# Performance work log

Measured on AMD Instinct MI355X. Metric: run time of the kernel, lower is better.

The kernel has to match this reference:

```python
import jax, jax.numpy as jnp
import numpy as np


def setup_inputs() -> dict:
    key = jax.random.key(0)
    k1, k2, k3 = jax.random.split(key, 3)
    x = jax.random.normal(k1, (32, 256, 56, 56), dtype=jnp.float32)
    att_w = jax.random.normal(k2, (4, 256), dtype=jnp.float32) * 0.05  # 1x1 attention conv weight (K, Cin)
    weight = jax.random.normal(k3, (4, 256, 256, 3, 3), dtype=jnp.float32) * 0.05  # (K, Cout, Cin, kh, kw)
    return {"x": x, "att_w": att_w, "weight": weight}


def reference(x, att_w, weight):
    # x: (B, Cin, H, W); att_w: (K, Cin); weight: (K, Cout, Cin, kh, kw)
    # Attention: global avg pool -> 1x1 conv (Cin->K) -> sigmoid  (named softmax_att but is sigmoid)
    pooled = jnp.mean(x, axis=(2, 3))                 # (B, Cin)
    att = jax.nn.sigmoid(pooled @ att_w.T)            # (B, K)
    # Per-sample expert-mixed conv kernels
    agg_w = jnp.einsum('bk,koihw->boihw', att, weight)  # (B, Cout, Cin, kh, kw)

    def conv_one(xi, wi):
        # xi: (Cin, H, W), wi: (Cout, Cin, kh, kw)
        return jax.lax.conv_general_dilated(
            xi[None], wi,
            window_strides=(1, 1),
            padding=[(1, 1), (1, 1)],
            rhs_dilation=(1, 1),
            dimension_numbers=('NCHW', 'OIHW', 'NCHW'),
        )[0]

    out = jax.vmap(conv_one)(x, agg_w)                # (B, Cout, H, W)
    return out
```

## Files before the change

kernel.cpp:

```cpp
#include <hip/hip_runtime.h>

typedef __attribute__((ext_vector_type(8))) short short8;
typedef __attribute__((ext_vector_type(4))) float floatx4;

__device__ __forceinline__ unsigned short bf16_rne(float f) {
  unsigned int u = __builtin_bit_cast(unsigned int, f);
  u += 0x7fffu + ((u >> 16) & 1u);
  return (unsigned short)(u >> 16);
}

__device__ __forceinline__ void glds16(const void* g, void* l) {
  __builtin_amdgcn_global_load_lds((const __attribute__((address_space(1))) void*)g,
                                   (__attribute__((address_space(3))) void*)l, 16, 0, 0);
}


__global__ void zero_pk_kernel(float* __restrict__ pk) {
  pk[threadIdx.x] = 0.f;
}

__global__ __launch_bounds__(256) void prep_kernel(const float* __restrict__ x,
                                                   const float* __restrict__ att_w,
                                                   unsigned short* __restrict__ xpad,
                                                   float* __restrict__ pooledk) {
  const int bid = blockIdx.x;
  const int b   = bid / 196;
  const int rem = bid - b * 196;
  const int cig = rem / 49;
  const int spc = rem - cig * 49;
  const int t  = threadIdx.x;
  const int cs = t >> 6, sl = t & 63;
  const int sp0 = spc * 64;

  __shared__ unsigned short T2[64 * 72];
  __shared__ float red[4][4];

  const float* xrow = x + (size_t)(b * 256 + cig * 64 + cs * 16) * 3136 + sp0 + sl;
  float v[16];
  #pragma unroll
  for (int i = 0; i < 16; ++i) v[i] = xrow[(size_t)i * 3136];

  float acc0 = 0.f, acc1 = 0.f, acc2 = 0.f, acc3 = 0.f;
  #pragma unroll
  for (int i = 0; i < 16; ++i) {
    const int ci = cig * 64 + cs * 16 + i;
    acc0 += v[i] * att_w[0 * 256 + ci];
    acc1 += v[i] * att_w[1 * 256 + ci];
    acc2 += v[i] * att_w[2 * 256 + ci];
    acc3 += v[i] * att_w[3 * 256 + ci];
  }
  #pragma unroll
  for (int o = 32; o > 0; o >>= 1) {
    acc0 += __shfl_xor(acc0, o, 64);
    acc1 += __shfl_xor(acc1, o, 64);
    acc2 += __shfl_xor(acc2, o, 64);
    acc3 += __shfl_xor(acc3, o, 64);
  }
  if (sl == 0) { red[cs][0] = acc0; red[cs][1] = acc1; red[cs][2] = acc2; red[cs][3] = acc3; }

  short8 w0, w1;
  #pragma unroll
  for (int i = 0; i < 8; ++i) w0[i] = (short)bf16_rne(v[i]);
  #pragma unroll
  for (int i = 0; i < 8; ++i) w1[i] = (short)bf16_rne(v[8 + i]);
  *(short8*)(T2 + sl * 72 + cs * 16) = w0;
  *(short8*)(T2 + sl * 72 + cs * 16 + 8) = w1;
  __syncthreads();

  if (t < 4) {
    float s = red[0][t] + red[1][t] + red[2][t] + red[3][t];
    atomicAdd(&pooledk[b * 4 + t], s);
  }

  unsigned short* xb = xpad + (size_t)b * (8 * 3364 * 32);
  #pragma unroll
  for (int it = 0; it < 2; ++it) {
    const int c9 = it * 256 + t;
    const int o2 = c9 & 3, spl = (c9 >> 2) & 63, kcsel = c9 >> 8;
    const int kc = cig * 2 + kcsel;
    const int spg = sp0 + spl;
    const int h = spg / 56, wc = spg - h * 56;
    const int pos = (h + 1) * 58 + (wc + 1);
    const short8 vv = *(const short8*)(T2 + spl * 72 + (kcsel * 4 + o2) * 8);
    *(short8*)(xb + (size_t)kc * (3364 * 32) + pos * 32 + o2 * 8) = vv;
  }

  if (cig == 0 && spc < 4) {
    const short8 z = {0, 0, 0, 0, 0, 0, 0, 0};
    #pragma unroll
    for (int it = 0; it < 8; ++it) {
      const int idx = it * 256 + t;
      if (idx >= 1824) break;
      const int s8 = idx & 3, kc = (idx >> 2) & 7, j = idx >> 5;
      const int pi = spc * 57 + j;
      int h2, w2;
      if (pi < 58)       { h2 = 0;  w2 = pi; }
      else if (pi < 116) { h2 = 57; w2 = pi - 58; }
      else { const int k = pi - 116; h2 = 1 + (k >> 1); w2 = (k & 1) * 57; }
      *(short8*)(xb + (size_t)kc * (3364 * 32) + (h2 * 58 + w2) * 32 + s8 * 8) = z;
    }
  }
}

__global__ __launch_bounds__(256) void agg_kernel(const float* __restrict__ w,
                                                  const float* __restrict__ pooledk,
                                                  unsigned short* __restrict__ agg) {
  const int co = blockIdx.x;
  const int bq = blockIdx.y;
  const int t = threadIdx.x;
  __shared__ float W[4][2304];
  __shared__ float attl[16];
  if (t < 16) {
    const float z = pooledk[bq * 16 + t] * (1.f / 3136.f);
    attl[t] = 1.f / (1.f + expf(-z));
  }
  #pragma unroll
  for (int e = 0; e < 4; ++e) {
    const float* src = w + (size_t)(e * 256 + co) * 2304;
    #pragma unroll
    for (int j = 0; j < 9; ++j) W[e][j * 256 + t] = src[j * 256 + t];
  }
  __syncthreads();

  #pragma unroll
  for (int rep = 0; rep < 2; ++rep) {
    const int id = rep * 256 + t;
    if (id < 288) {
      const int kc  = id / 36;
      const int rm  = id - kc * 36;
      const int rs  = rm >> 2;
      const int oct = rm & 3;
      const int wib = (kc * 32 + oct * 8) * 9 + rs;
      const int off = (kc * 9 + rs) * 8192 + co * 32 + oct * 8;
      float w0[8], w1[8], w2[8], w3[8];
      #pragma unroll
      for (int u = 0; u < 8; ++u) {
        w0[u] = W[0][wib + u * 9];
        w1[u] = W[1][wib + u * 9];
        w2[u] = W[2][wib + u * 9];
        w3[u] = W[3][wib + u * 9];
      }
      #pragma unroll
      for (int bl = 0; bl < 4; ++bl) {
        const int b = bq * 4 + bl;
        const float a0 = attl[bl * 4 + 0], a1 = attl[bl * 4 + 1];
        const float a2 = attl[bl * 4 + 2], a3 = attl[bl * 4 + 3];
        short8 vv;
        #pragma unroll
        for (int u = 0; u < 8; ++u)
          vv[u] = (short)bf16_rne(a0 * w0[u] + a1 * w1[u] + a2 * w2[u] + a3 * w3[u]);
        *(short8*)(agg + (size_t)b * 589824 + off) = vv;
      }
    }
  }
}

__device__ __forceinline__ void stageB(const unsigned short* __restrict__ xkc,
                                       unsigned short* Bs, int oh_min, int t) {
  #pragma unroll
  for (int i = 0; i < 6; ++i) {
    const int c = i * 256 + t;
    if (c < 1392) {
      const int pos = c >> 2, sub = c & 3;
      const int prow = pos / 58;
      const int pcol = pos - prow * 58;
      int ih2 = oh_min + prow; if (ih2 > 57) ih2 = 57;
      glds16(xkc + ((size_t)(ih2 * 58 + pcol) * 32 + sub * 8), (void*)(Bs + c * 8));
    }
  }
}

__global__ __launch_bounds__(256, 3) void conv_kernel(const unsigned short* __restrict__ xpad,
                                                      const unsigned short* __restrict__ aggw,
                                                      float* __restrict__ out) {
  __shared__ alignas(16) unsigned short Bsm[2][348 * 32];

  const int t  = threadIdx.x;
  const int bx0 = blockIdx.x;
  const int bx  = (bx0 & 7) * 200 + (bx0 >> 3);
  const int p_t  = bx % 25;
  const int co_t = (bx / 25) & 1;
  const int b    = bx / 50;
  const int p0   = p_t * 128;
  const int oh_min = p0 / 56;

  const unsigned short* xb  = xpad + (size_t)b * (8 * 3364 * 32);
  const unsigned short* awb = aggw + (size_t)b * 589824 + co_t * 4096;

  const int lane = t & 63;
  const int wv = t >> 6;
  const int wm = wv >> 1;
  const int wn = wv & 1;
  const int m16 = lane & 15;
  const int q = lane >> 4;

  int aoff[4], brow[4];
  #pragma unroll
  for (int i = 0; i < 4; ++i)
    aoff[i] = (wm * 64 + i * 16 + m16) * 32 + q * 8;
  #pragma unroll
  for (int j = 0; j < 4; ++j) {
    const int pf = p0 + wn * 64 + j * 16 + m16;
    const int oh = pf / 56;
    const int ow = pf - oh * 56;
    brow[j] = ((oh - oh_min) * 58 + ow) * 32 + q * 8;
  }

  floatx4 acc[4][4];
  #pragma unroll
  for (int i = 0; i < 4; ++i)
    #pragma unroll
    for (int j = 0; j < 4; ++j)
      acc[i][j] = (floatx4){0.f, 0.f, 0.f, 0.f};

  stageB(xb, Bsm[0], oh_min, t);
  __syncthreads();

  for (int kc = 0; kc < 8; ++kc) {
    const unsigned short* Bcur = Bsm[kc & 1];
    if (kc < 7)
      stageB(xb + (size_t)(kc + 1) * (3364 * 32), Bsm[(kc + 1) & 1], oh_min, t);

    const unsigned short* aslab = awb + (size_t)kc * 9 * 8192;
    #pragma unroll
    for (int rs = 0; rs < 9; ++rs) {
      const int r = rs / 3, s = rs - r * 3;
      const int d = (r * 58 + s) * 32;
      short8 af[4], bfr[4];
      #pragma unroll
      for (int i = 0; i < 4; ++i)
        af[i] = *(const short8*)(aslab + (size_t)rs * 8192 + aoff[i]);
      #pragma unroll
      for (int j = 0; j < 4; ++j)
        bfr[j] = *(const short8*)(Bcur + brow[j] + d);
      #pragma unroll
      for (int i = 0; i < 4; ++i)
        #pragma unroll
        for (int j = 0; j < 4; ++j)
          acc[i][j] = __builtin_amdgcn_mfma_f32_16x16x32_bf16(af[i], bfr[j], acc[i][j], 0, 0, 0);
    }
    __syncthreads();
  }

  #pragma unroll
  for (int i = 0; i < 4; ++i) {
    const int co = co_t * 128 + wm * 64 + i * 16 + q * 4;
    float* orow = out + (size_t)(b * 256 + co) * 3136;
    #pragma unroll
    for (int j = 0; j < 4; ++j) {
      const int pp = p0 + wn * 64 + j * 16 + m16;
      if (pp < 3136) {
        #pragma unroll
        for (int rg = 0; rg < 4; ++rg)
          orow[(size_t)rg * 3136 + pp] = acc[i][j][rg];
      }
    }
  }
}

extern "C" void kernel_launch(void* const* d_in, const int* in_sizes, int n_in,
                              void* d_out, int out_size, void* d_ws, size_t ws_size,
                              hipStream_t stream) {
  const float* x      = (const float*)d_in[0];
  const float* att_w  = (const float*)d_in[1];
  const float* weight = (const float*)d_in[2];
  float* out = (float*)d_out;

  char* ws = (char*)d_ws;
  float* pooledk       = (float*)ws;
  unsigned short* agg  = (unsigned short*)(ws + 65536);
  unsigned short* xpad = (unsigned short*)(ws + 65536 + 37748736);

  zero_pk_kernel<<<1, 128, 0, stream>>>(pooledk);
  prep_kernel<<<6272, 256, 0, stream>>>(x, att_w, xpad, pooledk);
  agg_kernel<<<dim3(256, 8), 256, 0, stream>>>(weight, pooledk, agg);
  conv_kernel<<<1600, 256, 0, stream>>>(xpad, agg, out);
}
```

Before: 366.5 us.

## Software-pipeline A-fragment loads and interleave B staging across rs iterations

Precomputes the per-thread global offsets for staging the input tile once, outside the channel loop. Each of the six async global-to-LDS copies for the next chunk is now issued inside one of the first six rs iterations rather than all at the start. The weight fragments for iteration rs+1 are prefetched from global memory while the MFMAs for rs run, and the MFMA block is raised in wave priority with s_setprio. Scheduling barriers hold this order in place. The aim is to hide global load latency behind the matrix math, at the cost of extra registers for the prefetch buffers and offsets.

```diff
diff --git a/kernel.cpp b/kernel.cpp
--- a/kernel.cpp
+++ b/kernel.cpp
@@ -155,21 +155,6 @@
   }
 }
 
-__device__ __forceinline__ void stageB(const unsigned short* __restrict__ xkc,
-                                       unsigned short* Bs, int oh_min, int t) {
-  #pragma unroll
-  for (int i = 0; i < 6; ++i) {
-    const int c = i * 256 + t;
-    if (c < 1392) {
-      const int pos = c >> 2, sub = c & 3;
-      const int prow = pos / 58;
-      const int pcol = pos - prow * 58;
-      int ih2 = oh_min + prow; if (ih2 > 57) ih2 = 57;
-      glds16(xkc + ((size_t)(ih2 * 58 + pcol) * 32 + sub * 8), (void*)(Bs + c * 8));
-    }
-  }
-}
-
 __global__ __launch_bounds__(256, 3) void conv_kernel(const unsigned short* __restrict__ xpad,
                                                       const unsigned short* __restrict__ aggw,
                                                       float* __restrict__ out) {
@@ -206,6 +191,18 @@
     brow[j] = ((oh - oh_min) * 58 + ow) * 32 + q * 8;
   }
 
+  int bofO[6];
+  #pragma unroll
+  for (int i = 0; i < 6; ++i) {
+    const int c = i * 256 + t;
+    if (c < 1392) {
+      const int pos = c >> 2, sub = c & 3;
+      const int prow = pos / 58, pcol = pos - prow * 58;
+      int ih2 = oh_min + prow; if (ih2 > 57) ih2 = 57;
+      bofO[i] = (ih2 * 58 + pcol) * 32 + sub * 8;
+    } else bofO[i] = -1;
+  }
+
   floatx4 acc[4][4];
   #pragma unroll
   for (int i = 0; i < 4; ++i)
@@ -213,31 +210,53 @@
     for (int j = 0; j < 4; ++j)
       acc[i][j] = (floatx4){0.f, 0.f, 0.f, 0.f};
 
-  stageB(xb, Bsm[0], oh_min, t);
+  #pragma unroll
+  for (int i = 0; i < 6; ++i)
+    if (bofO[i] >= 0) glds16(xb + bofO[i], (void*)(Bsm[0] + (i * 256 + t) * 8));
   __syncthreads();
 
   for (int kc = 0; kc < 8; ++kc) {
     const unsigned short* Bcur = Bsm[kc & 1];
-    if (kc < 7)
-      stageB(xb + (size_t)(kc + 1) * (3364 * 32), Bsm[(kc + 1) & 1], oh_min, t);
-
-    const unsigned short* aslab = awb + (size_t)kc * 9 * 8192;
+    unsigned short* Bnxt = Bsm[(kc + 1) & 1];
+    const unsigned short* xnxt = xb + (size_t)(kc + 1) * (3364 * 32);
+    const unsigned short* aslab = awb + (size_t)kc * 73728;
+    const bool doB = (kc < 7);
+
+    short8 afc[4], afn[4];
+    #pragma unroll
+    for (int i = 0; i < 4; ++i)
+      afc[i] = *(const short8*)(aslab + aoff[i]);
+
     #pragma unroll
     for (int rs = 0; rs < 9; ++rs) {
+      if (rs < 8) {
+        #pragma unroll
+        for (int i = 0; i < 4; ++i)
+          afn[i] = *(const short8*)(aslab + (size_t)(rs + 1) * 8192 + aoff[i]);
+      }
+      __builtin_amdgcn_sched_barrier(0);
+      if (rs < 6 && doB && bofO[rs] >= 0)
+        glds16(xnxt + bofO[rs], (void*)(Bnxt + (rs * 256 + t) * 8));
+      __builtin_amdgcn_sched_barrier(0);
+
       const int r = rs / 3, s = rs - r * 3;
       const int d = (r * 58 + s) * 32;
-      short8 af[4], bfr[4];
-      #pragma unroll
-      for (int i = 0; i < 4; ++i)
-        af[i] = *(const short8*)(aslab + (size_t)rs * 8192 + aoff[i]);
+      short8 bfr[4];
       #pragma unroll
       for (int j = 0; j < 4; ++j)
         bfr[j] = *(const short8*)(Bcur + brow[j] + d);
+      __builtin_amdgcn_s_setprio(1);
       #pragma unroll
       for (int i = 0; i < 4; ++i)
         #pragma unroll
         for (int j = 0; j < 4; ++j)
-          acc[i][j] = __builtin_amdgcn_mfma_f32_16x16x32_bf16(af[i], bfr[j], acc[i][j], 0, 0, 0);
+          acc[i][j] = __builtin_amdgcn_mfma_f32_16x16x32_bf16(afc[i], bfr[j], acc[i][j], 0, 0, 0);
+      __builtin_amdgcn_s_setprio(0);
+
+      if (rs < 8) {
+        #pragma unroll
+        for (int i = 0; i < 4; ++i) afc[i] = afn[i];
+      }
     }
     __syncthreads();
   }
```

Result: faster. 337.7 us (-7.9%).
